# Kernel tuning notes

Measured on AMD Instinct MI355X. Metric: run time of the kernel, lower is better.

## Reference

```python
import jax, jax.numpy as jnp
import numpy as np

N = 100000   # nodes
E = 1600000  # edges (avg degree 16)
D = 256      # in_channels == dim (forward hard-codes BatchNorm1d(256))
BN_EPS = 1e-5


def _batchnorm(x, gamma, beta):
    # training-mode BatchNorm1d: batch statistics over node dim, biased variance
    mu = jnp.mean(x, axis=0)
    var = jnp.var(x, axis=0)
    return (x - mu) * jax.lax.rsqrt(var + BN_EPS) * gamma + beta


def _gin_conv(x, src, dst, n, W1, b1, gamma, beta, W2, b2):
    # GINConv, eps=0: nn((1+eps)*x + sum_{j in N(i)} x_j)
    agg = jax.ops.segment_sum(x[src], dst, num_segments=n)  # sparse neighbor sum
    h = x + agg
    h = jax.nn.relu(_batchnorm(h @ W1 + b1, gamma, beta))
    return jax.nn.relu(h @ W2 + b2)


def setup_inputs() -> dict:
    key = jax.random.key(0)
    ks = jax.random.split(key, 8)
    x = jax.random.normal(ks[0], (N, D), dtype=jnp.float32)
    edge_index = jax.random.randint(ks[1], (2, E), 0, N, dtype=jnp.int64)
    s = 0.02
    inp = {
        "x": x,
        "edge_index": edge_index,
        # fresh BatchNorm1d(256) in forward (default affine params)
        "g0": jnp.ones((D,), jnp.float32),
        "b0": jnp.zeros((D,), jnp.float32),
        # conv1 MLP: Linear-BN-ReLU-Linear-ReLU
        "W1a": jax.random.normal(ks[2], (D, D), jnp.float32) * s,
        "b1a": jnp.zeros((D,), jnp.float32),
        "g1": jnp.ones((D,), jnp.float32),
        "bt1": jnp.zeros((D,), jnp.float32),
        "W1b": jax.random.normal(ks[3], (D, D), jnp.float32) * s,
        "b1b": jnp.zeros((D,), jnp.float32),
        # conv2 MLP
        "W2a": jax.random.normal(ks[4], (D, D), jnp.float32) * s,
        "b2a": jnp.zeros((D,), jnp.float32),
        "g2": jnp.ones((D,), jnp.float32),
        "bt2": jnp.zeros((D,), jnp.float32),
        "W2b": jax.random.normal(ks[5], (D, D), jnp.float32) * s,
        "b2b": jnp.zeros((D,), jnp.float32),
    }
    return inp


def reference(x, edge_index, g0, b0, W1a, b1a, g1, bt1, W1b, b1b,
              W2a, b2a, g2, bt2, W2b, b2b):
    n = x.shape[0]
    src, dst = edge_index[0], edge_index[1]
    h = _batchnorm(x, g0, b0)                       # fresh BN(256) on input
    h = _gin_conv(h, src, dst, n, W1a, b1a, g1, bt1, W1b, b1b)
    h = jax.nn.relu(h)                              # outer relu (dropout=eval, identity)
    h = _gin_conv(h, src, dst, n, W2a, b2a, g2, bt2, W2b, b2b)
    return jax.nn.relu(h)
```

## Files before the change

kernel.cpp:

```cpp
#include <hip/hip_runtime.h>

#define N_NODES 100000
#define N_EDGES 1600000
#define DIM 256
#define NBINS 196
#define BINCAP 16384

typedef unsigned short bf16u;
typedef __attribute__((ext_vector_type(8))) short bf16x8s;
typedef __attribute__((ext_vector_type(4))) float f32x4;

__device__ __forceinline__ float bf2f(unsigned int u16) {
    union { unsigned int i; float f; } x; x.i = u16 << 16; return x.f;
}
__device__ __forceinline__ float hi2f(unsigned int u) {
    union { unsigned int i; float f; } x; x.i = u & 0xffff0000u; return x.f;
}
__device__ __forceinline__ float lo2f(unsigned int u) {
    union { unsigned int i; float f; } x; x.i = u << 16; return x.f;
}
__device__ __forceinline__ bf16u f2bf(float f) {
    union { float f; unsigned int i; } x; x.f = f;
    unsigned int i = x.i;
    return (bf16u)((i + 0x7fffu + ((i >> 16) & 1u)) >> 16);
}
__device__ __forceinline__ float loadv(const void* p, size_t i, int isf32) {
    return isf32 ? ((const float*)p)[i] : bf2f(((const bf16u*)p)[i]);
}
__device__ __forceinline__ void async_copy16(const void* g, void* l) {
    __builtin_amdgcn_global_load_lds((const __attribute__((address_space(1))) void*)g,
                                     (__attribute__((address_space(3))) void*)l, 16, 0, 0);
}

__global__ void detect_flags(const unsigned* xw, const int* ei, int* flags, int* gBinFill,
                             float* sums) {
    __shared__ int cnt, nz;
    if (threadIdx.x == 0) { cnt = 0; nz = 0; }
    __syncthreads();
    gBinFill[threadIdx.x] = 0;
#pragma unroll
    for (int i = 0; i < 6; ++i) sums[i * 256 + threadIdx.x] = 0.f;
    unsigned u = xw[threadIdx.x];
    float av = fabsf(bf2f(u & 0xffffu));
    if (av > 1e-5f && av < 50.f) atomicAdd(&cnt, 1);
    if (ei[2 * threadIdx.x + 1] != 0) atomicAdd(&nz, 1);
    __syncthreads();
    if (threadIdx.x == 0) {
        flags[0] = (cnt >= 128) ? 0 : 1;
        if (nz == 0) { flags[1] = 2; flags[2] = 2 * N_EDGES; }
        else         { flags[1] = 1; flags[2] = N_EDGES; }
    }
}

__global__ void transpose_w(const void* W0, const void* W1, const void* W2, const void* W3,
                            bf16u* Wt, const int* flags) {
    __shared__ bf16u tile[64][65];
    int isf32 = flags[0];
    const void* W = (blockIdx.y == 0) ? W0 : (blockIdx.y == 1) ? W1 : (blockIdx.y == 2) ? W2 : W3;
    bf16u* out = Wt + (size_t)blockIdx.y * DIM * DIM;
    int t = threadIdx.x;
    int tx = t & 63, ty = t >> 6;
    int k0 = (blockIdx.x >> 2) * 64, n0 = (blockIdx.x & 3) * 64;
#pragma unroll
    for (int i = 0; i < 16; ++i) {
        int r = ty + i * 4;
        tile[tx][r] = f2bf(loadv(W, (size_t)(k0 + r) * DIM + (n0 + tx), isf32));
    }
    __syncthreads();
#pragma unroll
    for (int i = 0; i < 16; ++i) {
        int r = ty + i * 4;
        out[(size_t)(n0 + r) * DIM + (k0 + tx)] = tile[r][tx];
    }
}

__global__ __launch_bounds__(256) void bin_scatter(const int* __restrict__ ei,
                                                   const int* __restrict__ flags,
                                                   uint2* __restrict__ gRec,
                                                   int* __restrict__ gBinFill) {
    __shared__ int cnt[256];
    __shared__ int cur[256];
    __shared__ uint2 rec[4096];
    int t = threadIdx.x;
    cnt[t] = 0; cur[t] = 0;
    __syncthreads();
    int st = flags[1], ofs = flags[2];
    int e0 = blockIdx.x * 4096;
#pragma unroll
    for (int i = 0; i < 16; ++i) {
        int e = e0 + i * 256 + t;
        uint2 r;
        if (e < N_EDGES) {
            r.x = (unsigned)ei[(size_t)ofs + (size_t)e * st];
            r.y = (unsigned)ei[(size_t)e * st];
            atomicAdd(&cnt[r.x >> 9], 1);
        } else {
            r.x = 0xffffffffu; r.y = 0;
        }
        rec[i * 256 + t] = r;
    }
    __syncthreads();
    if (t < NBINS) {
        int c = cnt[t];
        int b = (c > 0) ? atomicAdd(&gBinFill[t], c) : 0;
        cnt[t] = b;
    }
    __syncthreads();
#pragma unroll
    for (int i = 0; i < 16; ++i) {
        uint2 r = rec[i * 256 + t];
        if (r.x != 0xffffffffu) {
            int b = r.x >> 9;
            int li = atomicAdd(&cur[b], 1);
            int pos = cnt[b] + li;
            if (pos < BINCAP) gRec[(size_t)b * BINCAP + pos] = r;
        }
    }
}

__global__ void bin_scan(const int* gBinFill, int* binBase) {
    __shared__ int s[256];
    int t = threadIdx.x;
    s[t] = (t < NBINS) ? gBinFill[t] : 0;
    __syncthreads();
    for (int off = 1; off < 256; off <<= 1) {
        int v = (t >= off) ? s[t - off] : 0;
        __syncthreads();
        s[t] += v;
        __syncthreads();
    }
    binBase[t + 1] = s[t];
    if (t == 0) binBase[0] = 0;
}

__global__ __launch_bounds__(256) void bin_csr(const uint2* __restrict__ gRec,
                                               const int* __restrict__ gBinFill,
                                               const int* __restrict__ binBase,
                                               int* __restrict__ rp, int* __restrict__ col) {
    __shared__ int cntA[512], scanB[512], noff[512], ncur[512];
    int bin = blockIdx.x, t = threadIdx.x;
    int cnt = gBinFill[bin];
    if (cnt > BINCAP) cnt = BINCAP;
    int gbase = binBase[bin], lo = bin << 9;
    cntA[t] = 0; cntA[t + 256] = 0; ncur[t] = 0; ncur[t + 256] = 0;
    __syncthreads();
    const uint2* R = gRec + (size_t)bin * BINCAP;
    for (int j = t; j < cnt; j += 256) atomicAdd(&cntA[(int)R[j].x - lo], 1);
    __syncthreads();
    scanB[t] = cntA[t]; scanB[t + 256] = cntA[t + 256];
    __syncthreads();
    for (int off = 1; off < 512; off <<= 1) {
        int v0 = (t >= off) ? scanB[t - off] : 0;
        int v1 = (t + 256 >= off) ? scanB[t + 256 - off] : 0;
        __syncthreads();
        scanB[t] += v0; scanB[t + 256] += v1;
        __syncthreads();
    }
    noff[t] = scanB[t] - cntA[t];
    noff[t + 256] = scanB[t + 256] - cntA[t + 256];
    __syncthreads();
    int n0 = lo + t, n1 = lo + t + 256;
    if (n0 < N_NODES) rp[n0] = gbase + noff[t];
    if (n1 < N_NODES) rp[n1] = gbase + noff[t + 256];
    if (bin == 0 && t == 0) rp[N_NODES] = N_EDGES;
    for (int j = t; j < cnt; j += 256) {
        uint2 r = R[j];
        int k = (int)r.x - lo;
        int li = atomicAdd(&ncur[k], 1);
        col[gbase + noff[k] + li] = (int)r.y;
    }
}

__global__ void col_stats(const void* X, int nrows, float* sums, const int* flags, int dual) {
    __shared__ float ls[512];
    int isf32 = dual ? flags[0] : 0;
    int t = threadIdx.x;
    ls[t] = 0.f; ls[t + 256] = 0.f;
    __syncthreads();
    int rpb = (nrows + gridDim.x - 1) / gridDim.x;
    int r0 = blockIdx.x * rpb;
    int r1 = r0 + rpb; if (r1 > nrows) r1 = nrows;
    int cg = (t & 31) * 8;
    float s[8], q[8];
#pragma unroll
    for (int j = 0; j < 8; ++j) { s[j] = 0.f; q[j] = 0.f; }
    if (isf32) {
        for (int r = r0 + (t >> 5); r < r1; r += 8) {
            const float* xp = (const float*)X + (size_t)r * DIM + cg;
            f32x4 a = *(const f32x4*)xp, b = *(const f32x4*)(xp + 4);
#pragma unroll
            for (int j = 0; j < 4; ++j) {
                s[j] += a[j]; q[j] += a[j] * a[j];
                s[4 + j] += b[j]; q[4 + j] += b[j] * b[j];
            }
        }
    } else {
        for (int r = r0 + (t >> 5); r < r1; r += 8) {
            size_t base = (size_t)r * DIM + cg;
#pragma unroll
            for (int j = 0; j < 8; ++j) {
                float f = bf2f(((const bf16u*)X)[base + j]);
                s[j] += f; q[j] += f * f;
            }
        }
    }
#pragma unroll
    for (int j = 0; j < 8; ++j) {
        atomicAdd(&ls[cg + j], s[j]);
        atomicAdd(&ls[256 + cg + j], q[j]);
    }
    __syncthreads();
    atomicAdd(&sums[t], ls[t]);
    atomicAdd(&sums[256 + t], ls[256 + t]);
}

__global__ void bn_finalize(const float* sums, const void* gamma, const void* beta,
                            float* sc, float* sh, float inv_n, const int* flags) {
    int isf32 = flags[0];
    int t = threadIdx.x;
    float mu = sums[t] * inv_n;
    float var = sums[256 + t] * inv_n - mu * mu;
    float rs = rsqrtf(var + 1e-5f);
    float g = loadv(gamma, t, isf32), b = loadv(beta, t, isf32);
    sc[t] = rs * g;
    sh[t] = b - mu * rs * g;
}

__global__ void bn_apply(const void* X, const float* sc, const float* sh, bf16u* Y,
                         const int* flags, int dual, int relu) {
    int isf32 = dual ? flags[0] : 0;
    size_t i = (size_t)blockIdx.x * 256 + threadIdx.x;
    int c = ((int)(i & 31)) * 8;
    size_t base = i * 8;
    float v[8];
    if (isf32) {
        f32x4 x0 = *(const f32x4*)((const float*)X + base);
        f32x4 x1 = *(const f32x4*)((const float*)X + base + 4);
#pragma unroll
        for (int j = 0; j < 4; ++j) { v[j] = x0[j]; v[4 + j] = x1[j]; }
    } else {
        uint4 u = *(const uint4*)((const bf16u*)X + base);
        v[0] = lo2f(u.x); v[1] = hi2f(u.x);
        v[2] = lo2f(u.y); v[3] = hi2f(u.y);
        v[4] = lo2f(u.z); v[5] = hi2f(u.z);
        v[6] = lo2f(u.w); v[7] = hi2f(u.w);
    }
    f32x4 s0 = *(const f32x4*)(sc + c), s1 = *(const f32x4*)(sc + c + 4);
    f32x4 h0 = *(const f32x4*)(sh + c), h1 = *(const f32x4*)(sh + c + 4);
    float y[8];
#pragma unroll
    for (int j = 0; j < 4; ++j) {
        y[j]     = v[j]     * s0[j] + h0[j];
        y[4 + j] = v[4 + j] * s1[j] + h1[j];
    }
    if (relu) {
#pragma unroll
        for (int j = 0; j < 8; ++j) y[j] = fmaxf(y[j], 0.f);
    }
    uint4 ov;
    ov.x = (unsigned)f2bf(y[0]) | ((unsigned)f2bf(y[1]) << 16);
    ov.y = (unsigned)f2bf(y[2]) | ((unsigned)f2bf(y[3]) << 16);
    ov.z = (unsigned)f2bf(y[4]) | ((unsigned)f2bf(y[5]) << 16);
    ov.w = (unsigned)f2bf(y[6]) | ((unsigned)f2bf(y[7]) << 16);
    *(uint4*)(Y + base) = ov;
}

__global__ __launch_bounds__(256) void aggregate(const bf16u* __restrict__ h,
                                                 const int* __restrict__ rp,
                                                 const int* __restrict__ col,
                                                 bf16u* __restrict__ out) {
    int node = blockIdx.x * 4 + (threadIdx.x >> 6);
    int lane = threadIdx.x & 63;
    int p = lane >> 5, c = lane & 31;
    const uint4* hv = (const uint4*)h;
    float acc[8];
    if (p == 0) {
        uint4 u = hv[(size_t)node * 32 + c];
        acc[0] = lo2f(u.x); acc[1] = hi2f(u.x);
        acc[2] = lo2f(u.y); acc[3] = hi2f(u.y);
        acc[4] = lo2f(u.z); acc[5] = hi2f(u.z);
        acc[6] = lo2f(u.w); acc[7] = hi2f(u.w);
    } else {
#pragma unroll
        for (int j = 0; j < 8; ++j) acc[j] = 0.f;
    }
    int e = rp[node], e1 = rp[node + 1];
    for (; e + 8 <= e1; e += 8) {
        int s0 = col[e + p], s1 = col[e + 2 + p], s2 = col[e + 4 + p], s3 = col[e + 6 + p];
        uint4 a = hv[(size_t)s0 * 32 + c];
        uint4 b = hv[(size_t)s1 * 32 + c];
        uint4 d = hv[(size_t)s2 * 32 + c];
        uint4 f = hv[(size_t)s3 * 32 + c];
        acc[0] += lo2f(a.x); acc[1] += hi2f(a.x); acc[2] += lo2f(a.y); acc[3] += hi2f(a.y);
        acc[4] += lo2f(a.z); acc[5] += hi2f(a.z); acc[6] += lo2f(a.w); acc[7] += hi2f(a.w);
        acc[0] += lo2f(b.x); acc[1] += hi2f(b.x); acc[2] += lo2f(b.y); acc[3] += hi2f(b.y);
        acc[4] += lo2f(b.z); acc[5] += hi2f(b.z); acc[6] += lo2f(b.w); acc[7] += hi2f(b.w);
        acc[0] += lo2f(d.x); acc[1] += hi2f(d.x); acc[2] += lo2f(d.y); acc[3] += hi2f(d.y);
        acc[4] += lo2f(d.z); acc[5] += hi2f(d.z); acc[6] += lo2f(d.w); acc[7] += hi2f(d.w);
        acc[0] += lo2f(f.x); acc[1] += hi2f(f.x); acc[2] += lo2f(f.y); acc[3] += hi2f(f.y);
        acc[4] += lo2f(f.z); acc[5] += hi2f(f.z); acc[6] += lo2f(f.w); acc[7] += hi2f(f.w);
    }
    for (; e + 4 <= e1; e += 4) {
        int s0 = col[e + p], s1 = col[e + 2 + p];
        uint4 a = hv[(size_t)s0 * 32 + c];
        uint4 b = hv[(size_t)s1 * 32 + c];
        acc[0] += lo2f(a.x); acc[1] += hi2f(a.x); acc[2] += lo2f(a.y); acc[3] += hi2f(a.y);
        acc[4] += lo2f(a.z); acc[5] += hi2f(a.z); acc[6] += lo2f(a.w); acc[7] += hi2f(a.w);
        acc[0] += lo2f(b.x); acc[1] += hi2f(b.x); acc[2] += lo2f(b.y); acc[3] += hi2f(b.y);
        acc[4] += lo2f(b.z); acc[5] += hi2f(b.z); acc[6] += lo2f(b.w); acc[7] += hi2f(b.w);
    }
    for (; e < e1; e += 2) {
        int idx = e + p;
        if (idx < e1) {
            uint4 a = hv[(size_t)col[idx] * 32 + c];
            acc[0] += lo2f(a.x); acc[1] += hi2f(a.x); acc[2] += lo2f(a.y); acc[3] += hi2f(a.y);
            acc[4] += lo2f(a.z); acc[5] += hi2f(a.z); acc[6] += lo2f(a.w); acc[7] += hi2f(a.w);
        }
    }
#pragma unroll
    for (int j = 0; j < 8; ++j) acc[j] += __shfl_xor(acc[j], 32);
    if (p == 0) {
        uint4 ov;
        ov.x = (unsigned)f2bf(acc[0]) | ((unsigned)f2bf(acc[1]) << 16);
        ov.y = (unsigned)f2bf(acc[2]) | ((unsigned)f2bf(acc[3]) << 16);
        ov.z = (unsigned)f2bf(acc[4]) | ((unsigned)f2bf(acc[5]) << 16);
        ov.w = (unsigned)f2bf(acc[6]) | ((unsigned)f2bf(acc[7]) << 16);
        ((uint4*)out)[(size_t)node * 32 + c] = ov;
    }
}

__global__ __launch_bounds__(256) void gemm_bias(const bf16u* __restrict__ A,
                                                 const bf16u* __restrict__ Wt,
                                                 const void* __restrict__ bias,
                                                 void* __restrict__ Cout, int mrows,
                                                 const int* __restrict__ flags,
                                                 int relu, int f32out,
                                                 float* __restrict__ stats,
                                                 const float* __restrict__ bnsc,
                                                 const float* __restrict__ bnsh) {
    __shared__ bf16u As[2][128 * 64];
    __shared__ bf16u Bs[2][128 * 64];
    __shared__ float lsum[256];
    int isf32 = flags[0];
    int t = threadIdx.x;
    int w = t >> 6, lane = t & 63;
    int lr = lane & 15, lq = lane >> 4;
    int wm = w >> 1, wn = w & 1;
    int xcd = blockIdx.x & 7, j0 = blockIdx.x >> 3;
    int wkid = ((xcd < 4) ? xcd * 196 : 784 + (xcd - 4) * 195) + j0;
    int rowBase = (wkid >> 1) * 128, colBase = (wkid & 1) * 128;
    f32x4 acc[4][4] = {};
    lsum[t] = 0.f;
    int srow = t >> 3;
    int g8   = ((t & 7) ^ ((t >> 3) & 7)) * 8;
    int ldsOff = (t >> 3) * 64 + (t & 7) * 8;

    if (bnsc) {
        f32x4 s0v = *(const f32x4*)(bnsc + g8);
        f32x4 s1v = *(const f32x4*)(bnsc + g8 + 4);
        f32x4 h0v = *(const f32x4*)(bnsh + g8);
        f32x4 h1v = *(const f32x4*)(bnsh + g8 + 4);
#pragma unroll
        for (int p = 0; p < 4; ++p) {
            int r = p * 32 + srow;
            int gr = rowBase + r; gr = (gr < mrows) ? gr : (mrows - 1);
            uint4 av = *(const uint4*)(A + (size_t)gr * 256 + g8);
            uint4 ov;
            ov.x = (unsigned)f2bf(fmaxf(lo2f(av.x) * s0v[0] + h0v[0], 0.f)) |
                   ((unsigned)f2bf(fmaxf(hi2f(av.x) * s0v[1] + h0v[1], 0.f)) << 16);
            ov.y = (unsigned)f2bf(fmaxf(lo2f(av.y) * s0v[2] + h0v[2], 0.f)) |
                   ((unsigned)f2bf(fmaxf(hi2f(av.y) * s0v[3] + h0v[3], 0.f)) << 16);
            ov.z = (unsigned)f2bf(fmaxf(lo2f(av.z) * s1v[0] + h1v[0], 0.f)) |
                   ((unsigned)f2bf(fmaxf(hi2f(av.z) * s1v[1] + h1v[1], 0.f)) << 16);
            ov.w = (unsigned)f2bf(fmaxf(lo2f(av.w) * s1v[2] + h1v[2], 0.f)) |
                   ((unsigned)f2bf(fmaxf(hi2f(av.w) * s1v[3] + h1v[3], 0.f)) << 16);
            *(uint4*)&As[0][p * 2048 + ldsOff] = ov;
            async_copy16(Wt + (size_t)(colBase + r) * 256 + g8, &Bs[0][(p * 32 + (w << 3)) * 64]);
        }
    } else {
#pragma unroll
        for (int p = 0; p < 4; ++p) {
            int r = p * 32 + srow;
            int gr = rowBase + r; gr = (gr < mrows) ? gr : (mrows - 1);
            async_copy16(A + (size_t)gr * 256 + g8, &As[0][(p * 32 + (w << 3)) * 64]);
            async_copy16(Wt + (size_t)(colBase + r) * 256 + g8, &Bs[0][(p * 32 + (w << 3)) * 64]);
        }
    }

    for (int kt = 0; kt < 4; ++kt) {
        int b = kt & 1, bn = b ^ 1;
        int kn = (kt + 1) * 64;
        __syncthreads();
        uint4 av[4];
        if (kt < 3) {
            if (bnsc) {
#pragma unroll
                for (int p = 0; p < 4; ++p) {
                    int r = p * 32 + srow;
                    int gr = rowBase + r; gr = (gr < mrows) ? gr : (mrows - 1);
                    av[p] = *(const uint4*)(A + (size_t)gr * 256 + kn + g8);
                }
#pragma unroll
                for (int p = 0; p < 4; ++p) {
                    int r = p * 32 + srow;
                    async_copy16(Wt + (size_t)(colBase + r) * 256 + kn + g8,
                                 &Bs[bn][(p * 32 + (w << 3)) * 64]);
                }
            } else {
#pragma unroll
                for (int p = 0; p < 4; ++p) {
                    int r = p * 32 + srow;
                    int gr = rowBase + r; gr = (gr < mrows) ? gr : (mrows - 1);
                    async_copy16(A + (size_t)gr * 256 + kn + g8,
                                 &As[bn][(p * 32 + (w << 3)) * 64]);
                    async_copy16(Wt + (size_t)(colBase + r) * 256 + kn + g8,
                                 &Bs[bn][(p * 32 + (w << 3)) * 64]);
                }
            }
        }
#pragma unroll
        for (int ks = 0; ks < 2; ++ks) {
            bf16x8s af[4], bfv[4];
#pragma unroll
            for (int mt = 0; mt < 4; ++mt) {
                int ar = wm * 64 + mt * 16 + lr;
                af[mt] = *(const bf16x8s*)&As[b][ar * 64 + (((ks * 4 + lq) ^ (lr & 7)) * 8)];
            }
#pragma unroll
            for (int nt = 0; nt < 4; ++nt) {
                int br = wn * 64 + nt * 16 + lr;
                bfv[nt] = *(const bf16x8s*)&Bs[b][br * 64 + (((ks * 4 + lq) ^ (lr & 7)) * 8)];
            }
#pragma unroll
            for (int mt = 0; mt < 4; ++mt)
#pragma unroll
                for (int nt = 0; nt < 4; ++nt)
                    acc[mt][nt] = __builtin_amdgcn_mfma_f32_16x16x32_bf16(af[mt], bfv[nt], acc[mt][nt], 0, 0, 0);
        }
        if (bnsc && kt < 3) {
            f32x4 s0v = *(const f32x4*)(bnsc + kn + g8);
            f32x4 s1v = *(const f32x4*)(bnsc + kn + g8 + 4);
            f32x4 h0v = *(const f32x4*)(bnsh + kn + g8);
            f32x4 h1v = *(const f32x4*)(bnsh + kn + g8 + 4);
#pragma unroll
            for (int p = 0; p < 4; ++p) {
                uint4 ov;
                ov.x = (unsigned)f2bf(fmaxf(lo2f(av[p].x) * s0v[0] + h0v[0], 0.f)) |
                       ((unsigned)f2bf(fmaxf(hi2f(av[p].x) * s0v[1] + h0v[1], 0.f)) << 16);
                ov.y = (unsigned)f2bf(fmaxf(lo2f(av[p].y) * s0v[2] + h0v[2], 0.f)) |
                       ((unsigned)f2bf(fmaxf(hi2f(av[p].y) * s0v[3] + h0v[3], 0.f)) << 16);
                ov.z = (unsigned)f2bf(fmaxf(lo2f(av[p].z) * s1v[0] + h1v[0], 0.f)) |
                       ((unsigned)f2bf(fmaxf(hi2f(av[p].z) * s1v[1] + h1v[1], 0.f)) << 16);
                ov.w = (unsigned)f2bf(fmaxf(lo2f(av[p].w) * s1v[2] + h1v[2], 0.f)) |
                       ((unsigned)f2bf(fmaxf(hi2f(av[p].w) * s1v[3] + h1v[3], 0.f)) << 16);
                *(uint4*)&As[bn][p * 2048 + ldsOff] = ov;
            }
        }
    }

    int storef32 = f32out && isf32;
#pragma unroll
    for (int nt = 0; nt < 4; ++nt) {
        int cl = wn * 64 + nt * 16 + lr;
        int c = colBase + cl;
        float bv = loadv(bias, c, isf32);
        float ssum = 0.f, ssq = 0.f;
#pragma unroll
        for (int mt = 0; mt < 4; ++mt) {
            int r0 = rowBase + wm * 64 + mt * 16 + lq * 4;
#pragma unroll
            for (int j = 0; j < 4; ++j) {
                int r = r0 + j;
                if (r < mrows) {
                    float y = acc[mt][nt][j] + bv;
                    if (relu) y = fmaxf(y, 0.f);
                    if (storef32) ((float*)Cout)[(size_t)r * 256 + c] = y;
                    else          ((bf16u*)Cout)[(size_t)r * 256 + c] = f2bf(y);
                    ssum += y; ssq += y * y;
                }
            }
        }
        if (stats) {
            atomicAdd(&lsum[cl], ssum);
            atomicAdd(&lsum[128 + cl], ssq);
        }
    }
    if (stats) {
        __syncthreads();
        if (t < 128) {
            atomicAdd(&stats[colBase + t], lsum[t]);
            atomicAdd(&stats[256 + colBase + t], lsum[128 + t]);
        }
    }
}

extern "C" void kernel_launch(void* const* d_in, const int* in_sizes, int n_in,
                              void* d_out, int out_size, void* d_ws, size_t ws_size,
                              hipStream_t stream) {
    const void* x   = d_in[0];
    const int*  ei  = (const int*)d_in[1];
    const void* g0  = d_in[2];
    const void* b0  = d_in[3];
    const void* W1a = d_in[4];
    const void* b1a = d_in[5];
    const void* g1  = d_in[6];
    const void* bt1 = d_in[7];
    const void* W1b = d_in[8];
    const void* b1b = d_in[9];
    const void* W2a = d_in[10];
    const void* b2a = d_in[11];
    const void* g2  = d_in[12];
    const void* bt2 = d_in[13];
    const void* W2b = d_in[14];
    const void* b2b = d_in[15];

    char* ws = (char*)d_ws;
    size_t off = 0;
    auto alloc = [&](size_t bytes) {
        char* p = ws + off;
        off += (bytes + 255) & ~(size_t)255;
        return p;
    };
    const size_t FB = (size_t)N_NODES * DIM * 2;
    bf16u* bufA  = (bf16u*)alloc(FB);
    bf16u* bufB  = (bf16u*)alloc(FB);
    bf16u* Wt    = (bf16u*)alloc((size_t)4 * DIM * DIM * 2);
    int*   colA  = (int*)alloc((size_t)N_EDGES * 4);
    int*   rp    = (int*)alloc((size_t)(N_NODES + 1) * 4);
    int*   gBinFill = (int*)alloc(256 * 4);
    int*   binBase  = (int*)alloc(260 * 4);
    float* sums0 = (float*)alloc(512 * 4);
    float* sums1 = (float*)alloc(512 * 4);
    float* sums2 = (float*)alloc(512 * 4);
    float* sc    = (float*)alloc(256 * 4);
    float* sh    = (float*)alloc(256 * 4);
    int*   flags = (int*)alloc(4 * 4);

    uint2* gRec = (uint2*)bufB;

    bf16u* Wt1a = Wt;
    bf16u* Wt1b = Wt + 65536;
    bf16u* Wt2a = Wt + 2 * 65536;
    bf16u* Wt2b = Wt + 3 * 65536;

    const float inv_n = 1.0f / (float)N_NODES;

    detect_flags<<<1, 256, 0, stream>>>((const unsigned*)x, ei, flags, gBinFill, sums0);
    transpose_w<<<dim3(16, 4), 256, 0, stream>>>(W1a, W1b, W2a, W2b, Wt, flags);

    bin_scatter<<<391, 256, 0, stream>>>(ei, flags, gRec, gBinFill);
    bin_scan<<<1, 256, 0, stream>>>(gBinFill, binBase);
    bin_csr<<<NBINS, 256, 0, stream>>>(gRec, gBinFill, binBase, rp, colA);

    col_stats<<<500, 256, 0, stream>>>(x, N_NODES, sums0, flags, 1);
    bn_finalize<<<1, 256, 0, stream>>>(sums0, g0, b0, sc, sh, inv_n, flags);
    bn_apply<<<12500, 256, 0, stream>>>(x, sc, sh, bufB, flags, 1, 0);

    aggregate<<<25000, 256, 0, stream>>>(bufB, rp, colA, bufA);
    gemm_bias<<<1564, 256, 0, stream>>>(bufA, Wt1a, b1a, bufB, N_NODES, flags, 0, 0, sums1,
                                        nullptr, nullptr);
    bn_finalize<<<1, 256, 0, stream>>>(sums1, g1, bt1, sc, sh, inv_n, flags);
    gemm_bias<<<1564, 256, 0, stream>>>(bufB, Wt1b, b1b, bufA, N_NODES, flags, 1, 0, nullptr,
                                        sc, sh);

    aggregate<<<25000, 256, 0, stream>>>(bufA, rp, colA, bufB);
    gemm_bias<<<1564, 256, 0, stream>>>(bufB, Wt2a, b2a, bufA, N_NODES, flags, 0, 0, sums2,
                                        nullptr, nullptr);
    bn_finalize<<<1, 256, 0, stream>>>(sums2, g2, bt2, sc, sh, inv_n, flags);
    gemm_bias<<<1564, 256, 0, stream>>>(bufA, Wt2b, b2b, d_out, N_NODES, flags, 1, 1, nullptr,
                                        sc, sh);
}
```

Baseline: 824.8 us.

## Fuse neighbor aggregation with first GEMM and BN stats in one kernel

```diff
diff --git a/kernel.cpp b/kernel.cpp
--- a/kernel.cpp
+++ b/kernel.cpp
@@ -265,67 +265,146 @@
     *(uint4*)(Y + base) = ov;
 }
 
-__global__ __launch_bounds__(256) void aggregate(const bf16u* __restrict__ h,
-                                                 const int* __restrict__ rp,
-                                                 const int* __restrict__ col,
-                                                 bf16u* __restrict__ out) {
-    int node = blockIdx.x * 4 + (threadIdx.x >> 6);
-    int lane = threadIdx.x & 63;
-    int p = lane >> 5, c = lane & 31;
-    const uint4* hv = (const uint4*)h;
-    float acc[8];
-    if (p == 0) {
-        uint4 u = hv[(size_t)node * 32 + c];
-        acc[0] = lo2f(u.x); acc[1] = hi2f(u.x);
-        acc[2] = lo2f(u.y); acc[3] = hi2f(u.y);
-        acc[4] = lo2f(u.z); acc[5] = hi2f(u.z);
-        acc[6] = lo2f(u.w); acc[7] = hi2f(u.w);
-    } else {
-#pragma unroll
-        for (int j = 0; j < 8; ++j) acc[j] = 0.f;
-    }
-    int e = rp[node], e1 = rp[node + 1];
-    for (; e + 8 <= e1; e += 8) {
-        int s0 = col[e + p], s1 = col[e + 2 + p], s2 = col[e + 4 + p], s3 = col[e + 6 + p];
-        uint4 a = hv[(size_t)s0 * 32 + c];
-        uint4 b = hv[(size_t)s1 * 32 + c];
-        uint4 d = hv[(size_t)s2 * 32 + c];
-        uint4 f = hv[(size_t)s3 * 32 + c];
-        acc[0] += lo2f(a.x); acc[1] += hi2f(a.x); acc[2] += lo2f(a.y); acc[3] += hi2f(a.y);
-        acc[4] += lo2f(a.z); acc[5] += hi2f(a.z); acc[6] += lo2f(a.w); acc[7] += hi2f(a.w);
-        acc[0] += lo2f(b.x); acc[1] += hi2f(b.x); acc[2] += lo2f(b.y); acc[3] += hi2f(b.y);
-        acc[4] += lo2f(b.z); acc[5] += hi2f(b.z); acc[6] += lo2f(b.w); acc[7] += hi2f(b.w);
-        acc[0] += lo2f(d.x); acc[1] += hi2f(d.x); acc[2] += lo2f(d.y); acc[3] += hi2f(d.y);
-        acc[4] += lo2f(d.z); acc[5] += hi2f(d.z); acc[6] += lo2f(d.w); acc[7] += hi2f(d.w);
-        acc[0] += lo2f(f.x); acc[1] += hi2f(f.x); acc[2] += lo2f(f.y); acc[3] += hi2f(f.y);
-        acc[4] += lo2f(f.z); acc[5] += hi2f(f.z); acc[6] += lo2f(f.w); acc[7] += hi2f(f.w);
-    }
-    for (; e + 4 <= e1; e += 4) {
-        int s0 = col[e + p], s1 = col[e + 2 + p];
-        uint4 a = hv[(size_t)s0 * 32 + c];
-        uint4 b = hv[(size_t)s1 * 32 + c];
-        acc[0] += lo2f(a.x); acc[1] += hi2f(a.x); acc[2] += lo2f(a.y); acc[3] += hi2f(a.y);
-        acc[4] += lo2f(a.z); acc[5] += hi2f(a.z); acc[6] += lo2f(a.w); acc[7] += hi2f(a.w);
-        acc[0] += lo2f(b.x); acc[1] += hi2f(b.x); acc[2] += lo2f(b.y); acc[3] += hi2f(b.y);
-        acc[4] += lo2f(b.z); acc[5] += hi2f(b.z); acc[6] += lo2f(b.w); acc[7] += hi2f(b.w);
-    }
-    for (; e < e1; e += 2) {
-        int idx = e + p;
-        if (idx < e1) {
-            uint4 a = hv[(size_t)col[idx] * 32 + c];
-            acc[0] += lo2f(a.x); acc[1] += hi2f(a.x); acc[2] += lo2f(a.y); acc[3] += hi2f(a.y);
-            acc[4] += lo2f(a.z); acc[5] += hi2f(a.z); acc[6] += lo2f(a.w); acc[7] += hi2f(a.w);
-        }
-    }
-#pragma unroll
-    for (int j = 0; j < 8; ++j) acc[j] += __shfl_xor(acc[j], 32);
-    if (p == 0) {
-        uint4 ov;
-        ov.x = (unsigned)f2bf(acc[0]) | ((unsigned)f2bf(acc[1]) << 16);
-        ov.y = (unsigned)f2bf(acc[2]) | ((unsigned)f2bf(acc[3]) << 16);
-        ov.z = (unsigned)f2bf(acc[4]) | ((unsigned)f2bf(acc[5]) << 16);
-        ov.w = (unsigned)f2bf(acc[6]) | ((unsigned)f2bf(acc[7]) << 16);
-        ((uint4*)out)[(size_t)node * 32 + c] = ov;
+__global__ __launch_bounds__(512) void agg_gemm(const bf16u* __restrict__ h,
+                                                const int* __restrict__ rp,
+                                                const int* __restrict__ col,
+                                                const bf16u* __restrict__ Wt,
+                                                const void* __restrict__ bias,
+                                                bf16u* __restrict__ Cout,
+                                                const int* __restrict__ flags,
+                                                float* __restrict__ stats) {
+    __shared__ __align__(16) bf16u aggA[64 * 256];
+    __shared__ __align__(16) bf16u Bs[256 * 64];
+    __shared__ float lsum[512];
+    int isf32 = flags[0];
+    int t = threadIdx.x;
+    int w = t >> 6, lane = t & 63;
+    lsum[t] = 0.f;
+    int rb = blockIdx.x * 64;
+
+    {
+        int p = lane >> 5, c = lane & 31;
+        const uint4* hv = (const uint4*)h;
+        for (int i = 0; i < 8; ++i) {
+            int lrow = w * 8 + i;
+            int node = rb + lrow;
+            if (node >= N_NODES) node = N_NODES - 1;
+            float acc[8];
+            if (p == 0) {
+                uint4 u = hv[(size_t)node * 32 + c];
+                acc[0] = lo2f(u.x); acc[1] = hi2f(u.x);
+                acc[2] = lo2f(u.y); acc[3] = hi2f(u.y);
+                acc[4] = lo2f(u.z); acc[5] = hi2f(u.z);
+                acc[6] = lo2f(u.w); acc[7] = hi2f(u.w);
+            } else {
+#pragma unroll
+                for (int j = 0; j < 8; ++j) acc[j] = 0.f;
+            }
+            int e = rp[node], e1 = rp[node + 1];
+            for (; e + 8 <= e1; e += 8) {
+                int s0 = col[e + p], s1 = col[e + 2 + p], s2 = col[e + 4 + p], s3 = col[e + 6 + p];
+                uint4 a = hv[(size_t)s0 * 32 + c];
+                uint4 b = hv[(size_t)s1 * 32 + c];
+                uint4 d = hv[(size_t)s2 * 32 + c];
+                uint4 f = hv[(size_t)s3 * 32 + c];
+                acc[0] += lo2f(a.x); acc[1] += hi2f(a.x); acc[2] += lo2f(a.y); acc[3] += hi2f(a.y);
+                acc[4] += lo2f(a.z); acc[5] += hi2f(a.z); acc[6] += lo2f(a.w); acc[7] += hi2f(a.w);
+                acc[0] += lo2f(b.x); acc[1] += hi2f(b.x); acc[2] += lo2f(b.y); acc[3] += hi2f(b.y);
+                acc[4] += lo2f(b.z); acc[5] += hi2f(b.z); acc[6] += lo2f(b.w); acc[7] += hi2f(b.w);
+                acc[0] += lo2f(d.x); acc[1] += hi2f(d.x); acc[2] += lo2f(d.y); acc[3] += hi2f(d.y);
+                acc[4] += lo2f(d.z); acc[5] += hi2f(d.z); acc[6] += lo2f(d.w); acc[7] += hi2f(d.w);
+                acc[0] += lo2f(f.x); acc[1] += hi2f(f.x); acc[2] += lo2f(f.y); acc[3] += hi2f(f.y);
+                acc[4] += lo2f(f.z); acc[5] += hi2f(f.z); acc[6] += lo2f(f.w); acc[7] += hi2f(f.w);
+            }
+            for (; e + 4 <= e1; e += 4) {
+                int s0 = col[e + p], s1 = col[e + 2 + p];
+                uint4 a = hv[(size_t)s0 * 32 + c];
+                uint4 b = hv[(size_t)s1 * 32 + c];
+                acc[0] += lo2f(a.x); acc[1] += hi2f(a.x); acc[2] += lo2f(a.y); acc[3] += hi2f(a.y);
+                acc[4] += lo2f(a.z); acc[5] += hi2f(a.z); acc[6] += lo2f(a.w); acc[7] += hi2f(a.w);
+                acc[0] += lo2f(b.x); acc[1] += hi2f(b.x); acc[2] += lo2f(b.y); acc[3] += hi2f(b.y);
+                acc[4] += lo2f(b.z); acc[5] += hi2f(b.z); acc[6] += lo2f(b.w); acc[7] += hi2f(b.w);
+            }
+            for (; e < e1; e += 2) {
+                int idx = e + p;
+                if (idx < e1) {
+                    uint4 a = hv[(size_t)col[idx] * 32 + c];
+                    acc[0] += lo2f(a.x); acc[1] += hi2f(a.x); acc[2] += lo2f(a.y); acc[3] += hi2f(a.y);
+                    acc[4] += lo2f(a.z); acc[5] += hi2f(a.z); acc[6] += lo2f(a.w); acc[7] += hi2f(a.w);
+                }
+            }
+#pragma unroll
+            for (int j = 0; j < 8; ++j) acc[j] += __shfl_xor(acc[j], 32);
+            if (p == 0) {
+                uint4 ov;
+                ov.x = (unsigned)f2bf(acc[0]) | ((unsigned)f2bf(acc[1]) << 16);
+                ov.y = (unsigned)f2bf(acc[2]) | ((unsigned)f2bf(acc[3]) << 16);
+                ov.z = (unsigned)f2bf(acc[4]) | ((unsigned)f2bf(acc[5]) << 16);
+                ov.w = (unsigned)f2bf(acc[6]) | ((unsigned)f2bf(acc[7]) << 16);
+                *(uint4*)&aggA[lrow * 256 + ((c ^ (lrow & 7)) * 8)] = ov;
+            }
+        }
+    }
+
+    int lr = lane & 15, lq = lane >> 4;
+    int wm = w >> 2, wn = w & 3;
+    f32x4 acc[2][4] = {};
+    int srow = t >> 3;
+    int g8 = ((t & 7) ^ ((t >> 3) & 7)) * 8;
+    for (int kt = 0; kt < 4; ++kt) {
+        __syncthreads();
+#pragma unroll
+        for (int p = 0; p < 4; ++p)
+            async_copy16(Wt + (size_t)(p * 64 + srow) * 256 + kt * 64 + g8,
+                         &Bs[(p * 64 + (w << 3)) * 64]);
+        __syncthreads();
+#pragma unroll
+        for (int ks = 0; ks < 2; ++ks) {
+            bf16x8s af[2], bfv[4];
+#pragma unroll
+            for (int mt = 0; mt < 2; ++mt) {
+                int ar = wm * 32 + mt * 16 + lr;
+                int kc = kt * 8 + ks * 4 + lq;
+                af[mt] = *(const bf16x8s*)&aggA[ar * 256 + ((kc ^ (lr & 7)) * 8)];
+            }
+#pragma unroll
+            for (int nt = 0; nt < 4; ++nt) {
+                int br = wn * 64 + nt * 16 + lr;
+                bfv[nt] = *(const bf16x8s*)&Bs[br * 64 + (((ks * 4 + lq) ^ (lr & 7)) * 8)];
+            }
+#pragma unroll
+            for (int mt = 0; mt < 2; ++mt)
+#pragma unroll
+                for (int nt = 0; nt < 4; ++nt)
+                    acc[mt][nt] = __builtin_amdgcn_mfma_f32_16x16x32_bf16(af[mt], bfv[nt], acc[mt][nt], 0, 0, 0);
+        }
+    }
+
+#pragma unroll
+    for (int nt = 0; nt < 4; ++nt) {
+        int c = wn * 64 + nt * 16 + lr;
+        float bv = loadv(bias, c, isf32);
+        float ssum = 0.f, ssq = 0.f;
+#pragma unroll
+        for (int mt = 0; mt < 2; ++mt) {
+            int r0 = rb + wm * 32 + mt * 16 + lq * 4;
+#pragma unroll
+            for (int j = 0; j < 4; ++j) {
+                int r = r0 + j;
+                if (r < N_NODES) {
+                    float y = acc[mt][nt][j] + bv;
+                    Cout[(size_t)r * 256 + c] = f2bf(y);
+                    ssum += y; ssq += y * y;
+                }
+            }
+        }
+        atomicAdd(&lsum[c], ssum);
+        atomicAdd(&lsum[256 + c], ssq);
+    }
+    __syncthreads();
+    if (t < 256) {
+        atomicAdd(&stats[t], lsum[t]);
+        atomicAdd(&stats[256 + t], lsum[256 + t]);
     }
 }
 
@@ -464,7 +543,6 @@
         int cl = wn * 64 + nt * 16 + lr;
         int c = colBase + cl;
         float bv = loadv(bias, c, isf32);
-        float ssum = 0.f, ssq = 0.f;
 #pragma unroll
         for (int mt = 0; mt < 4; ++mt) {
             int r0 = rowBase + wm * 64 + mt * 16 + lq * 4;
@@ -476,22 +554,11 @@
                     if (relu) y = fmaxf(y, 0.f);
                     if (storef32) ((float*)Cout)[(size_t)r * 256 + c] = y;
                     else          ((bf16u*)Cout)[(size_t)r * 256 + c] = f2bf(y);
-                    ssum += y; ssq += y * y;
                 }
             }
         }
-        if (stats) {
-            atomicAdd(&lsum[cl], ssum);
-            atomicAdd(&lsum[128 + cl], ssq);
-        }
-    }
-    if (stats) {
-        __syncthreads();
-        if (t < 128) {
-            atomicAdd(&stats[colBase + t], lsum[t]);
-            atomicAdd(&stats[256 + colBase + t], lsum[128 + t]);
-        }
-    }
+    }
+    (void)stats;
 }
 
 extern "C" void kernel_launch(void* const* d_in, const int* in_sizes, int n_in,
@@ -556,16 +623,12 @@
     bn_finalize<<<1, 256, 0, stream>>>(sums0, g0, b0, sc, sh, inv_n, flags);
     bn_apply<<<12500, 256, 0, stream>>>(x, sc, sh, bufB, flags, 1, 0);
 
-    aggregate<<<25000, 256, 0, stream>>>(bufB, rp, colA, bufA);
-    gemm_bias<<<1564, 256, 0, stream>>>(bufA, Wt1a, b1a, bufB, N_NODES, flags, 0, 0, sums1,
-                                        nullptr, nullptr);
+    agg_gemm<<<1563, 512, 0, stream>>>(bufB, rp, colA, Wt1a, b1a, bufA, flags, sums1);
     bn_finalize<<<1, 256, 0, stream>>>(sums1, g1, bt1, sc, sh, inv_n, flags);
-    gemm_bias<<<1564, 256, 0, stream>>>(bufB, Wt1b, b1b, bufA, N_NODES, flags, 1, 0, nullptr,
+    gemm_bias<<<1564, 256, 0, stream>>>(bufA, Wt1b, b1b, bufB, N_NODES, flags, 1, 0, nullptr,
                                         sc, sh);
 
-    aggregate<<<25000, 256, 0, stream>>>(bufA, rp, colA, bufB);
-    gemm_bias<<<1564, 256, 0, stream>>>(bufB, Wt2a, b2a, bufA, N_NODES, flags, 0, 0, sums2,
-                                        nullptr, nullptr);
+    agg_gemm<<<1563, 512, 0, stream>>>(bufB, rp, colA, Wt2a, b2a, bufA, flags, sums2);
     bn_finalize<<<1, 256, 0, stream>>>(sums2, g2, bt2, sc, sh, inv_n, flags);
     gemm_bias<<<1564, 256, 0, stream>>>(bufA, Wt2b, b2b, d_out, N_NODES, flags, 1, 1, nullptr,
                                         sc, sh);
```

Result: faster. 798.7 us (-3.2%).
